# Optimization experiments

Hardware: AMD Instinct MI355X
Metric: run time of the kernel (lower is better)

Reference implementation:

```python
import jax, jax.numpy as jnp
import numpy as np

L, B, F, D = 12, 2048, 6144, 768

def setup_inputs() -> dict:
    key = jax.random.key(0)
    k1, k2, k3 = jax.random.split(key, 3)
    acts = jax.random.normal(k1, (L, B, F), dtype=jnp.float32)
    # decoder weights for target layer: stacked per source layer, [L, F, D]
    W = jax.random.normal(k2, (L, F, D), dtype=jnp.float32) * 0.02
    bias = jax.random.normal(k3, (L, D), dtype=jnp.float32) * 0.01
    return {"acts": acts, "W": W, "bias": bias, "layer_idx": 11}

def reference(acts, W, bias, layer_idx):
    # decode(): sum over src_layer <= layer_idx of Linear(a[src], W[src->tgt], b[src->tgt])
    n = layer_idx + 1  # static Python int -> static slice
    a = acts[:n]       # [n, B, F]
    w = W[:n]          # [n, F, D]
    b = bias[:n]       # [n, D]
    # fused accumulation of all per-source-layer GEMMs
    recon = jnp.einsum('lbf,lfd->bd', a, w) + jnp.sum(b, axis=0)  # [B, D]
    return recon
```

## Files before the change

kernel.cpp:

```cpp
#include <hip/hip_runtime.h>
#include <hip/hip_bf16.h>

#define NB 2048
#define NF 6144
#define ND 768
#define BM 256
#define BN 192
#define BK 64
#define SPLITK 2
#define KCH (NF / SPLITK)
#define NTIL (KCH / BK)

#define ABYTES (BM * 128)
#define BBYTES (BN * 128)
#define BUFB (ABYTES + BBYTES)

typedef __attribute__((ext_vector_type(4))) __bf16 bf16x4;
typedef __attribute__((ext_vector_type(8))) __bf16 bf16x8;
typedef __attribute__((ext_vector_type(4))) float f32x4;

__device__ __forceinline__ int fswz(int r) { return ((r & 7) ^ ((r >> 2) & 7)) & 7; }
__device__ __forceinline__ char* lds_addr(char* base, int row, int k) {
  const int blk = ((k >> 3) ^ fswz(row)) & 7;
  return base + row * 128 + (blk << 4) + ((k & 7) << 1);
}

__device__ __forceinline__ void async_ld16(void* lds, const void* g) {
  __builtin_amdgcn_global_load_lds(
      (const __attribute__((address_space(1))) void*)g,
      (__attribute__((address_space(3))) void*)lds, 16, 0, 0);
}

#define SBAR0() __builtin_amdgcn_sched_barrier(0)
#define LGKM(N)                                              \
  do {                                                       \
    asm volatile("s_waitcnt lgkmcnt(" #N ")" ::: "memory");  \
    SBAR0();                                                 \
  } while (0)
#define VMW(N)                                               \
  do {                                                       \
    asm volatile("s_waitcnt vmcnt(" #N ")" ::: "memory");    \
    SBAR0();                                                 \
  } while (0)

__global__ __launch_bounds__(256) void bias_init_kernel(
    const float* __restrict__ bias, const int* __restrict__ lidx,
    float* __restrict__ out) {
  int n = lidx[0] + 1;
  int i = blockIdx.x * 256 + threadIdx.x;
  if (i >= NB * ND) return;
  int d = i % ND;
  float s = 0.f;
  for (int l = 0; l < n; ++l) s += bias[l * ND + d];
  out[i] = s;
}

__global__ __launch_bounds__(256) void wt_kernel(
    const float* __restrict__ W, unsigned short* __restrict__ wt) {
  __shared__ float t[64][65];
  const int l = blockIdx.z, f0 = blockIdx.x * 64, d0 = blockIdx.y * 64;
  const int tid = threadIdx.x;
  const int fr = tid >> 4;
  const int dc4 = (tid & 15) * 4;
  const float* src = W + ((size_t)l * NF + f0 + fr) * ND + d0 + dc4;
#pragma unroll
  for (int i = 0; i < 4; ++i) {
    float4 v = *(const float4*)(src + (size_t)16 * i * ND);
    t[fr + 16 * i][dc4 + 0] = v.x;
    t[fr + 16 * i][dc4 + 1] = v.y;
    t[fr + 16 * i][dc4 + 2] = v.z;
    t[fr + 16 * i][dc4 + 3] = v.w;
  }
  __syncthreads();
  const int dr = tid >> 4;
  const int fc4 = (tid & 15) * 4;
  unsigned short* dst = wt + ((size_t)l * ND + d0 + dr) * NF + f0 + fc4;
#pragma unroll
  for (int i = 0; i < 4; ++i) {
    bf16x4 h;
    h[0] = (__bf16)t[fc4 + 0][dr + 16 * i];
    h[1] = (__bf16)t[fc4 + 1][dr + 16 * i];
    h[2] = (__bf16)t[fc4 + 2][dr + 16 * i];
    h[3] = (__bf16)t[fc4 + 3][dr + 16 * i];
    *(bf16x4*)(dst + (size_t)16 * i * NF) = h;
  }
}

__global__ __launch_bounds__(512, 2) void gemm_dma(
    const float* __restrict__ acts, const unsigned short* __restrict__ wt,
    const int* __restrict__ lidx, float* __restrict__ out, int nwg) {
  extern __shared__ char cbuf[];

  const int chunk = nwg >> 3;
  const int swz = (blockIdx.x & 7) * chunk + (blockIdx.x >> 3);
  const int by = swz & 3;
  int rem = swz >> 2;
  const int m = rem & 7; rem >>= 3;
  const int ks = rem & 1; rem >>= 1;
  const int l = rem;
  if (l > lidx[0]) return;

  const int brow = m * BM;
  const int ncol = by * BN;
  const int k0 = ks * KCH;

  const int tid = threadIdx.x;
  const int lane = tid & 63;
  const int wid = tid >> 6;
  const int wrow = (wid >> 1) * 64;
  const int wcol = (wid & 1) * 96;

  f32x4 acc[4][6];
#pragma unroll
  for (int i = 0; i < 4; ++i)
#pragma unroll
    for (int j = 0; j < 6; ++j) acc[i][j] = (f32x4){0.f, 0.f, 0.f, 0.f};

  const int s_arow = tid >> 3;
  const int s_ak = (tid & 7) * 8;
  const float* Aptr =
      acts + (size_t)l * NB * NF + (size_t)(brow + s_arow) * NF + k0 + s_ak;
  float4 av[4][2];

  const unsigned short* bSrc[3];
  int bDst[3];
#pragma unroll
  for (int j = 0; j < 3; ++j) {
    const int r0 = 8 * (3 * wid + j);
    const int r = r0 + (lane >> 3);
    const int ksl = (lane & 7) ^ fswz(r);
    bSrc[j] = wt + ((size_t)l * ND + ncol + r) * NF + k0 + ksl * 8;
    bDst[j] = ABYTES + r0 * 128;
  }

  auto ALOADS = [&](int kb) {
#pragma unroll
    for (int p = 0; p < 4; ++p) {
      av[p][0] = *(const float4*)(Aptr + (size_t)(64 * p) * NF + kb);
      av[p][1] = *(const float4*)(Aptr + (size_t)(64 * p) * NF + kb + 4);
    }
  };
  auto DMA_B = [&](int t, int buf) {
    char* b = cbuf + (size_t)buf * BUFB;
#pragma unroll
    for (int j = 0; j < 3; ++j)
      async_ld16(b + bDst[j], bSrc[j] + (size_t)t * BK);
  };
  auto ASTORE = [&](char* cA_) {
#pragma unroll
    for (int p = 0; p < 4; ++p) {
      bf16x8 h;
      h[0] = (__bf16)av[p][0].x; h[1] = (__bf16)av[p][0].y;
      h[2] = (__bf16)av[p][0].z; h[3] = (__bf16)av[p][0].w;
      h[4] = (__bf16)av[p][1].x; h[5] = (__bf16)av[p][1].y;
      h[6] = (__bf16)av[p][1].z; h[7] = (__bf16)av[p][1].w;
      *(bf16x8*)lds_addr(cA_, s_arow + 64 * p, s_ak) = h;
    }
  };

#define BF_READ(dst, P)                                                   \
  _Pragma("unroll") for (int ni = 0; ni < 2; ++ni)                        \
    _Pragma("unroll") for (int s = 0; s < 2; ++s)                         \
      dst[ni][s] = *(const bf16x8*)lds_addr(                              \
          rB, wcol + (2 * (P) + ni) * 16 + (lane & 15),                   \
          s * 32 + (lane >> 4) * 8);

#define MFMA16(bf, P)                                                     \
  __builtin_amdgcn_s_setprio(1);                                          \
  _Pragma("unroll") for (int s = 0; s < 2; ++s)                           \
    _Pragma("unroll") for (int mi = 0; mi < 4; ++mi)                      \
      _Pragma("unroll") for (int ni = 0; ni < 2; ++ni)                    \
        acc[mi][2 * (P) + ni] = __builtin_amdgcn_mfma_f32_16x16x32_bf16(  \
            aF[mi][s], bf[ni][s], acc[mi][2 * (P) + ni], 0, 0, 0);        \
  __builtin_amdgcn_s_setprio(0);                                          \
  SBAR0();

  ALOADS(0);
  DMA_B(0, 0);
  ASTORE(cbuf);
  VMW(0);
  LGKM(0);

  for (int t = 0; t < NTIL; ++t) {
    const int cur = t & 1;
    char* rA = cbuf + (size_t)cur * BUFB;
    char* rB = rA + ABYTES;
    char* wA = cbuf + (size_t)(cur ^ 1) * BUFB;
    const bool more = (t + 1 < NTIL);

    __builtin_amdgcn_s_barrier();
    SBAR0();

    if (more) {
      ALOADS((t + 1) * BK);
      DMA_B(t + 1, cur ^ 1);
    }
    SBAR0();

    bf16x8 aF[4][2];
#pragma unroll
    for (int mi = 0; mi < 4; ++mi)
#pragma unroll
      for (int s = 0; s < 2; ++s)
        aF[mi][s] = *(const bf16x8*)lds_addr(
            rA, wrow + mi * 16 + (lane & 15), s * 32 + (lane >> 4) * 8);
    bf16x8 bFa[2][2], bFb[2][2], bFc[2][2];
    BF_READ(bFa, 0)
    BF_READ(bFb, 1)
    SBAR0();
    LGKM(4);
    MFMA16(bFa, 0)

    BF_READ(bFc, 2)
    SBAR0();
    LGKM(4);
    MFMA16(bFb, 1)

    LGKM(0);
    MFMA16(bFc, 2)

    if (more) ASTORE(wA);
    VMW(0);
    LGKM(0);
  }

#undef BF_READ
#undef MFMA16

  const int orow = brow + wrow + ((lane >> 4) << 2);
  const int ocol = ncol + wcol + (lane & 15);
#pragma unroll
  for (int mi = 0; mi < 4; ++mi)
#pragma unroll
    for (int ni = 0; ni < 6; ++ni)
#pragma unroll
      for (int j = 0; j < 4; ++j)
        atomicAdd(out + (size_t)(orow + mi * 16 + j) * ND + (ocol + ni * 16),
                  acc[mi][ni][j]);
}

__global__ __launch_bounds__(512, 2) void gemm_fused(
    const float* __restrict__ acts, const float* __restrict__ W,
    const int* __restrict__ lidx, float* __restrict__ out, int nwg) {
  extern __shared__ char cbuf[];
  const int chunk = nwg >> 3;
  const int swz = (blockIdx.x & 7) * chunk + (blockIdx.x >> 3);
  const int by = swz & 3;
  int rem = swz >> 2;
  const int m = rem & 7; rem >>= 3;
  const int ks = rem & 1; rem >>= 1;
  const int l = rem;
  if (l > lidx[0]) return;
  const int brow = m * BM, ncol = by * BN, k0 = ks * KCH;
  const int tid = threadIdx.x, lane = tid & 63, wid = tid >> 6;
  const int wrow = (wid >> 1) * 64, wcol = (wid & 1) * 96;
  f32x4 acc[4][6];
#pragma unroll
  for (int i = 0; i < 4; ++i)
#pragma unroll
    for (int j = 0; j < 6; ++j) acc[i][j] = (f32x4){0.f, 0.f, 0.f, 0.f};
  const int s_arow = tid >> 3, s_ak = (tid & 7) * 8;
  const bool bstage = tid < 384;
  const int s_bd = (tid % 48) * 4, s_bk = (tid / 48) * 8;
  const float* Aptr =
      acts + (size_t)l * NB * NF + (size_t)(brow + s_arow) * NF + k0 + s_ak;
  const float* Bptr =
      W + (size_t)l * NF * ND + (size_t)(k0 + s_bk) * ND + (ncol + s_bd);
  float4 av[4][2]; float4 bv[8];
  auto LOADS = [&](int kb) {
#pragma unroll
    for (int p = 0; p < 4; ++p) {
      av[p][0] = *(const float4*)(Aptr + (size_t)(64 * p) * NF + kb);
      av[p][1] = *(const float4*)(Aptr + (size_t)(64 * p) * NF + kb + 4);
    }
    if (bstage) {
#pragma unroll
      for (int j = 0; j < 8; ++j)
        bv[j] = *(const float4*)(Bptr + (size_t)(kb + j) * ND);
    }
  };
  auto STORE = [&](char* cA_, char* cB_) {
#pragma unroll
    for (int p = 0; p < 4; ++p) {
      bf16x8 h;
      h[0] = (__bf16)av[p][0].x; h[1] = (__bf16)av[p][0].y;
      h[2] = (__bf16)av[p][0].z; h[3] = (__bf16)av[p][0].w;
      h[4] = (__bf16)av[p][1].x; h[5] = (__bf16)av[p][1].y;
      h[6] = (__bf16)av[p][1].z; h[7] = (__bf16)av[p][1].w;
      *(bf16x8*)lds_addr(cA_, s_arow + 64 * p, s_ak) = h;
    }
    if (bstage) {
#pragma unroll
      for (int dd = 0; dd < 4; ++dd) {
        bf16x8 h;
#pragma unroll
        for (int j = 0; j < 8; ++j) h[j] = (__bf16)bv[j][dd];
        *(bf16x8*)lds_addr(cB_, s_bd + dd, s_bk) = h;
      }
    }
  };
  LOADS(0);
  STORE(cbuf, cbuf + ABYTES);
  for (int t = 0; t < NTIL; ++t) {
    const int cur = t & 1;
    char* rA = cbuf + (size_t)cur * BUFB;
    char* rB = rA + ABYTES;
    char* wA = cbuf + (size_t)(cur ^ 1) * BUFB;
    char* wB = wA + ABYTES;
    LGKM(0);
    __builtin_amdgcn_s_barrier();
    SBAR0();
    if (t + 1 < NTIL) LOADS((t + 1) * BK);
    SBAR0();
    bf16x8 aF[4][2];
#pragma unroll
    for (int mi = 0; mi < 4; ++mi)
#pragma unroll
      for (int s = 0; s < 2; ++s)
        aF[mi][s] = *(const bf16x8*)lds_addr(
            rA, wrow + mi * 16 + (lane & 15), s * 32 + (lane >> 4) * 8);
#pragma unroll
    for (int p = 0; p < 3; ++p) {
      bf16x8 bF[2][2];
#pragma unroll
      for (int ni = 0; ni < 2; ++ni)
#pragma unroll
        for (int s = 0; s < 2; ++s)
          bF[ni][s] = *(const bf16x8*)lds_addr(
              rB, wcol + (2 * p + ni) * 16 + (lane & 15),
              s * 32 + (lane >> 4) * 8);
      LGKM(0);
      __builtin_amdgcn_s_setprio(1);
#pragma unroll
      for (int s = 0; s < 2; ++s)
#pragma unroll
        for (int mi = 0; mi < 4; ++mi)
#pragma unroll
          for (int ni = 0; ni < 2; ++ni)
            acc[mi][2 * p + ni] = __builtin_amdgcn_mfma_f32_16x16x32_bf16(
                aF[mi][s], bF[ni][s], acc[mi][2 * p + ni], 0, 0, 0);
      __builtin_amdgcn_s_setprio(0);
      SBAR0();
    }
    if (t + 1 < NTIL) STORE(wA, wB);
  }
  const int orow = brow + wrow + ((lane >> 4) << 2);
  const int ocol = ncol + wcol + (lane & 15);
#pragma unroll
  for (int mi = 0; mi < 4; ++mi)
#pragma unroll
    for (int ni = 0; ni < 6; ++ni)
#pragma unroll
      for (int j = 0; j < 4; ++j)
        atomicAdd(out + (size_t)(orow + mi * 16 + j) * ND + (ocol + ni * 16),
                  acc[mi][ni][j]);
}

extern "C" void kernel_launch(void* const* d_in, const int* in_sizes, int n_in,
                              void* d_out, int out_size, void* d_ws, size_t ws_size,
                              hipStream_t stream) {
  const float* acts = (const float*)d_in[0];
  const float* W    = (const float*)d_in[1];
  const float* bias = (const float*)d_in[2];
  const int*   lidx = (const int*)d_in[3];
  float* out = (float*)d_out;

  const int L = in_sizes[0] / (NB * NF);
  const int nwg = (ND / BN) * (NB / BM) * SPLITK * L;
  const size_t wsNeed = (size_t)L * NF * ND * 2;

  bias_init_kernel<<<dim3((NB * ND + 255) / 256), 256, 0, stream>>>(bias, lidx, out);

  if (ws_size >= wsNeed) {
    unsigned short* wsB = (unsigned short*)d_ws;
    wt_kernel<<<dim3(NF / 64, ND / 64, L), 256, 0, stream>>>(W, wsB);
    hipFuncSetAttribute((const void*)gemm_dma,
                        hipFuncAttributeMaxDynamicSharedMemorySize, 2 * BUFB);
    gemm_dma<<<dim3(nwg), 512, 2 * BUFB, stream>>>(acts, wsB, lidx, out, nwg);
  } else {
    hipFuncSetAttribute((const void*)gemm_fused,
                        hipFuncAttributeMaxDynamicSharedMemorySize, 2 * BUFB);
    gemm_fused<<<dim3(nwg), 512, 2 * BUFB, stream>>>(acts, W, lidx, out, nwg);
  }
}
```

Before: 542.7 us.

## Triple-buffer weight tiles and interleave loads with MFMA phases in main GEMM

The main GEMM now keeps the weight operand in three LDS buffers, prefetched two tiles ahead by async global-to-LDS loads, while activations stay double-buffered. Loads, stores and async DMA are spread across the three MFMA sub-phases, with barriers separating them, instead of being issued together at the top of each iteration. The aim is to hide global memory latency better. In exchange it uses more LDS per block (2*32KB + 3*24KB = 136KB), which may cut occupancy below two blocks per CU, and it adds eight barriers per iteration.

```diff
diff --git a/kernel.cpp b/kernel.cpp
--- a/kernel.cpp
+++ b/kernel.cpp
@@ -11,9 +11,10 @@
 #define KCH (NF / SPLITK)
 #define NTIL (KCH / BK)
 
-#define ABYTES (BM * 128)
-#define BBYTES (BN * 128)
-#define BUFB (ABYTES + BBYTES)
+#define A_BYTES (BM * 128)
+#define B_BYTES (BN * 128)
+#define BBUF_OFF (2 * A_BYTES)
+#define LDS_TOTAL (2 * A_BYTES + 3 * B_BYTES)
 
 typedef __attribute__((ext_vector_type(4))) __bf16 bf16x4;
 typedef __attribute__((ext_vector_type(8))) __bf16 bf16x8;
@@ -42,6 +43,11 @@
     asm volatile("s_waitcnt vmcnt(" #N ")" ::: "memory");    \
     SBAR0();                                                 \
   } while (0)
+#define BARRIER()                 \
+  do {                            \
+    __builtin_amdgcn_s_barrier(); \
+    SBAR0();                      \
+  } while (0)
 
 __global__ __launch_bounds__(256) void bias_init_kernel(
     const float* __restrict__ bias, const int* __restrict__ lidx,
@@ -86,7 +92,7 @@
   }
 }
 
-__global__ __launch_bounds__(512, 2) void gemm_dma(
+__global__ __launch_bounds__(512, 2) void gemm_sw(
     const float* __restrict__ acts, const unsigned short* __restrict__ wt,
     const int* __restrict__ lidx, float* __restrict__ out, int nwg) {
   extern __shared__ char cbuf[];
@@ -130,7 +136,7 @@
     const int r = r0 + (lane >> 3);
     const int ksl = (lane & 7) ^ fswz(r);
     bSrc[j] = wt + ((size_t)l * ND + ncol + r) * NF + k0 + ksl * 8;
-    bDst[j] = ABYTES + r0 * 128;
+    bDst[j] = r0 * 128;
   }
 
   auto ALOADS = [&](int kb) {
@@ -140,8 +146,8 @@
       av[p][1] = *(const float4*)(Aptr + (size_t)(64 * p) * NF + kb + 4);
     }
   };
-  auto DMA_B = [&](int t, int buf) {
-    char* b = cbuf + (size_t)buf * BUFB;
+  auto DMA_B = [&](int t) {
+    char* b = cbuf + BBUF_OFF + (size_t)(t % 3) * B_BYTES;
 #pragma unroll
     for (int j = 0; j < 3; ++j)
       async_ld16(b + bDst[j], bSrc[j] + (size_t)t * BK);
@@ -176,26 +182,19 @@
   SBAR0();
 
   ALOADS(0);
-  DMA_B(0, 0);
   ASTORE(cbuf);
+  DMA_B(0);
+  DMA_B(1);
   VMW(0);
   LGKM(0);
+  BARRIER();
 
   for (int t = 0; t < NTIL; ++t) {
-    const int cur = t & 1;
-    char* rA = cbuf + (size_t)cur * BUFB;
-    char* rB = rA + ABYTES;
-    char* wA = cbuf + (size_t)(cur ^ 1) * BUFB;
-    const bool more = (t + 1 < NTIL);
-
-    __builtin_amdgcn_s_barrier();
-    SBAR0();
-
-    if (more) {
-      ALOADS((t + 1) * BK);
-      DMA_B(t + 1, cur ^ 1);
-    }
-    SBAR0();
+    char* rA = cbuf + (size_t)(t & 1) * A_BYTES;
+    char* rB = cbuf + BBUF_OFF + (size_t)(t % 3) * B_BYTES;
+    char* wA = cbuf + (size_t)((t + 1) & 1) * A_BYTES;
+    const bool more1 = (t + 1 < NTIL);
+    const bool more2 = (t + 2 < NTIL);
 
     bf16x8 aF[4][2];
 #pragma unroll
@@ -204,24 +203,38 @@
       for (int s = 0; s < 2; ++s)
         aF[mi][s] = *(const bf16x8*)lds_addr(
             rA, wrow + mi * 16 + (lane & 15), s * 32 + (lane >> 4) * 8);
-    bf16x8 bFa[2][2], bFb[2][2], bFc[2][2];
-    BF_READ(bFa, 0)
-    BF_READ(bFb, 1)
-    SBAR0();
-    LGKM(4);
-    MFMA16(bFa, 0)
-
-    BF_READ(bFc, 2)
-    SBAR0();
-    LGKM(4);
-    MFMA16(bFb, 1)
-
-    LGKM(0);
-    MFMA16(bFc, 2)
-
-    if (more) ASTORE(wA);
-    VMW(0);
-    LGKM(0);
+    {
+      bf16x8 bF[2][2];
+      BF_READ(bF, 0)
+      if (more1) ALOADS((t + 1) * BK);
+      BARRIER();
+      LGKM(0);
+      MFMA16(bF, 0)
+      BARRIER();
+    }
+
+    {
+      bf16x8 bF[2][2];
+      BF_READ(bF, 1)
+      if (more2) DMA_B(t + 2);
+      BARRIER();
+      LGKM(0);
+      MFMA16(bF, 1)
+      BARRIER();
+    }
+
+    {
+      bf16x8 bF[2][2];
+      BF_READ(bF, 2)
+      if (more1) ASTORE(wA);
+      BARRIER();
+      LGKM(0);
+      MFMA16(bF, 2)
+      BARRIER();
+    }
+
+    if (more2) { VMW(3); } else { VMW(0); }
+    BARRIER();
   }
 
 #undef BF_READ
@@ -239,6 +252,7 @@
                   acc[mi][ni][j]);
 }
 
+#define F_BUF (A_BYTES + B_BYTES)
 __global__ __launch_bounds__(512, 2) void gemm_fused(
     const float* __restrict__ acts, const float* __restrict__ W,
     const int* __restrict__ lidx, float* __restrict__ out, int nwg) {
@@ -300,16 +314,15 @@
     }
   };
   LOADS(0);
-  STORE(cbuf, cbuf + ABYTES);
+  STORE(cbuf, cbuf + A_BYTES);
   for (int t = 0; t < NTIL; ++t) {
     const int cur = t & 1;
-    char* rA = cbuf + (size_t)cur * BUFB;
-    char* rB = rA + ABYTES;
-    char* wA = cbuf + (size_t)(cur ^ 1) * BUFB;
-    char* wB = wA + ABYTES;
+    char* rA = cbuf + (size_t)cur * F_BUF;
+    char* rB = rA + A_BYTES;
+    char* wA = cbuf + (size_t)(cur ^ 1) * F_BUF;
+    char* wB = wA + A_BYTES;
     LGKM(0);
-    __builtin_amdgcn_s_barrier();
-    SBAR0();
+    BARRIER();
     if (t + 1 < NTIL) LOADS((t + 1) * BK);
     SBAR0();
     bf16x8 aF[4][2];
@@ -374,12 +387,12 @@
   if (ws_size >= wsNeed) {
     unsigned short* wsB = (unsigned short*)d_ws;
     wt_kernel<<<dim3(NF / 64, ND / 64, L), 256, 0, stream>>>(W, wsB);
-    hipFuncSetAttribute((const void*)gemm_dma,
-                        hipFuncAttributeMaxDynamicSharedMemorySize, 2 * BUFB);
-    gemm_dma<<<dim3(nwg), 512, 2 * BUFB, stream>>>(acts, wsB, lidx, out, nwg);
+    hipFuncSetAttribute((const void*)gemm_sw,
+                        hipFuncAttributeMaxDynamicSharedMemorySize, LDS_TOTAL);
+    gemm_sw<<<dim3(nwg), 512, LDS_TOTAL, stream>>>(acts, wsB, lidx, out, nwg);
   } else {
     hipFuncSetAttribute((const void*)gemm_fused,
-                        hipFuncAttributeMaxDynamicSharedMemorySize, 2 * BUFB);
-    gemm_fused<<<dim3(nwg), 512, 2 * BUFB, stream>>>(acts, W, lidx, out, nwg);
-  }
-}
+                        hipFuncAttributeMaxDynamicSharedMemorySize, 2 * F_BUF);
+    gemm_fused<<<dim3(nwg), 512, 2 * F_BUF, stream>>>(acts, W, lidx, out, nwg);
+  }
+}
```

Result: faster. 498.3 us (-8.2%).
